# Optimization experiments

Measured on AMD Instinct MI355X. Metric: run time of the kernel, lower is better.

## Reference

```python
import jax, jax.numpy as jnp
import numpy as np

REL_SIZE = 65
TAG_SIZE = 4


def _rope(y):
    # Interleaved rotary position embedding, matching the torch module:
    # cos_pos = cos(theta) repeat_interleave(2), sin_pos = sin(theta) repeat_interleave(2)
    # y2 = (-y1, y0, -y3, y2, ...)
    B, S, H = y.shape
    half = H // 2
    pos = jnp.arange(S, dtype=jnp.float32)[:, None]                      # (S,1)
    inv_freq = jnp.power(10000.0, -2.0 * jnp.arange(half, dtype=jnp.float32) / H)
    theta = pos * inv_freq                                               # (S, half)
    cos = jnp.repeat(jnp.cos(theta), 2, axis=-1)                          # (S, H)
    sin = jnp.repeat(jnp.sin(theta), 2, axis=-1)                          # (S, H)
    yr = y.reshape(B, S, half, 2)
    y2 = jnp.stack([-yr[..., 1], yr[..., 0]], axis=-1).reshape(B, S, H)
    return y * cos + y2 * sin


def setup_inputs() -> dict:
    key = jax.random.key(0)
    k1, k2, k3 = jax.random.split(key, 3)
    B, S, H = 1, 160, 768
    y = jax.random.normal(k1, (B, S, H), dtype=jnp.float32)
    event_idx = jax.random.randint(k2, (B, 16), 0, S)
    W1 = jax.random.normal(k3, (H, 2 * H), dtype=jnp.float32) * 0.02
    b1 = jnp.zeros((H,), dtype=jnp.float32)
    W2 = jax.random.normal(jax.random.fold_in(key, 7), (REL_SIZE * TAG_SIZE, H), dtype=jnp.float32) * 0.02
    b2 = jnp.zeros((REL_SIZE * TAG_SIZE,), dtype=jnp.float32)
    return {"y": y, "event_idx": event_idx, "W1": W1, "b1": b1, "W2": W2, "b2": b2}


def reference(y, event_idx, W1, b1, W2, b2):
    # Eval path (training=False): event_idx unused, dropout = identity, sigmoid applied.
    B, S, H = y.shape
    yrot = _rope(y)
    # Linear(cat(a, b)) is separable: split W1 into the halves acting on a and b.
    Wa, Wb = W1[:, :H], W1[:, H:]
    left = jnp.einsum('bsh,oh->bso', yrot, Wa)                  # contribution of token i (row)
    right = jnp.einsum('bsh,oh->bso', yrot, Wb) + b1            # contribution of token j (col)
    h = jax.nn.relu(left[:, :, None, :] + right[:, None, :, :])  # (B, S, S, H)
    out = jnp.einsum('bijh,oh->bijo', h, W2) + b2               # (B, S, S, 260)
    out = out.reshape(B, S, S, REL_SIZE, TAG_SIZE).transpose(0, 3, 1, 2, 4)  # (B, 65, S, S, 4)
    return jax.nn.sigmoid(out)
```

## Files before the change

kernel.cpp:

```cpp
#include <hip/hip_runtime.h>
#include <hip/hip_bf16.h>
#include <cstdint>

#define SDIM 160
#define HDIM 768
#define HALF 384
#define ODIM 260
#define OPAD 272
#define CHUNK_BYTES 34816
#define WS_SMALL 1155088
#define WS_BIG   3514384

typedef __attribute__((ext_vector_type(8))) short short8;
typedef __attribute__((ext_vector_type(4))) float floatx4;
typedef _Float16 half8 __attribute__((ext_vector_type(8)));

typedef const __attribute__((address_space(1))) unsigned char gl_u8;
typedef __attribute__((address_space(3))) unsigned char lds_u8;

static __device__ __forceinline__ float bf2f(unsigned short u) {
    union { unsigned int i; float f; } v; v.i = ((unsigned int)u) << 16; return v.f;
}
static __device__ __forceinline__ unsigned short f2bf(float x) {
    __hip_bfloat16 h = __float2bfloat16(x);
    return *reinterpret_cast<unsigned short*>(&h);
}
static __device__ __forceinline__ unsigned short f2h(float x) {
    _Float16 h = (_Float16)x;
    return *reinterpret_cast<unsigned short*>(&h);
}
static __device__ __forceinline__ float q(float x) { return bf2f(f2bf(x)); }

__global__ __launch_bounds__(256) void prep_kernel(
    const float* __restrict__ y, const float* __restrict__ W1,
    const float* __restrict__ W2,
    unsigned short* __restrict__ yb, unsigned short* __restrict__ W2b,
    unsigned short* __restrict__ W1b, int do_w1b) {
    int bid = blockIdx.x;
    int t = threadIdx.x;
    if (bid < SDIM) {
        int s = bid;
        for (int p = t; p < HALF; p += 256) {
            float invf = __expf(-(2.0f * (float)p / (float)HDIM) * 9.210340371976184f);
            float th = (float)s * invf;
            float c = cosf(th), sn = sinf(th);
            float y0 = y[s * HDIM + 2 * p], y1 = y[s * HDIM + 2 * p + 1];
            yb[s * HDIM + 2 * p]     = f2bf(y0 * c - y1 * sn);
            yb[s * HDIM + 2 * p + 1] = f2bf(y1 * c + y0 * sn);
        }
    } else if (bid < SDIM + 102) {
        int idx = (bid - SDIM) * 256 + t;
        if (idx < 96 * OPAD) {
            int kg = idx / OPAD, row = idx - kg * OPAD;
            unsigned short o8[8];
            if (row < ODIM) {
                float4 a = *reinterpret_cast<const float4*>(W2 + row * HDIM + kg * 8);
                float4 b = *reinterpret_cast<const float4*>(W2 + row * HDIM + kg * 8 + 4);
                o8[0] = f2h(a.x); o8[1] = f2h(a.y); o8[2] = f2h(a.z); o8[3] = f2h(a.w);
                o8[4] = f2h(b.x); o8[5] = f2h(b.y); o8[6] = f2h(b.z); o8[7] = f2h(b.w);
            } else {
                #pragma unroll
                for (int e = 0; e < 8; ++e) o8[e] = 0;
            }
            *reinterpret_cast<uint4*>(W2b + ((size_t)kg * OPAD + row) * 8) =
                *reinterpret_cast<uint4*>(o8);
        }
    } else if (do_w1b) {
        int idx = (bid - SDIM - 102) * 256 + t;
        int kg = idx / 1536, row = idx - kg * 1536;
        const float* src = (row < 768) ? (W1 + row * 1536 + kg * 8)
                                       : (W1 + (row - 768) * 1536 + 768 + kg * 8);
        float4 a = *reinterpret_cast<const float4*>(src);
        float4 b = *reinterpret_cast<const float4*>(src + 4);
        unsigned short o8[8];
        o8[0] = f2bf(a.x); o8[1] = f2bf(a.y); o8[2] = f2bf(a.z); o8[3] = f2bf(a.w);
        o8[4] = f2bf(b.x); o8[5] = f2bf(b.y); o8[6] = f2bf(b.z); o8[7] = f2bf(b.w);
        *reinterpret_cast<uint4*>(W1b + ((size_t)kg * 1536 + row) * 8) =
            *reinterpret_cast<uint4*>(o8);
    }
}

__global__ __launch_bounds__(64, 2) void lr3_kernel(
    const unsigned short* __restrict__ yb, const unsigned short* __restrict__ W1b,
    const float* __restrict__ b1,
    unsigned short* __restrict__ Lb, unsigned short* __restrict__ Rt) {
    int l = threadIdx.x & 63;
    int l16 = l & 15, qd = l >> 4;
    int mt = blockIdx.x;
    int sq = blockIdx.y;
    int s0 = sq * 16 + l16;

    floatx4 acc = (floatx4){0.0f, 0.0f, 0.0f, 0.0f};

    const unsigned short* yrow0 = yb + s0 * HDIM;

    for (int ks = 0; ks < 24; ++ks) {
        int k = ks * 32 + qd * 8;
        int kg = ks * 4 + qd;
        union { uint4 u; short8 s; } bu0, au;
        bu0.u = *reinterpret_cast<const uint4*>(yrow0 + k);
        au.u = *reinterpret_cast<const uint4*>(
            W1b + ((size_t)kg * 1536 + mt * 16 + l16) * 8);
        acc = __builtin_amdgcn_mfma_f32_16x16x32_bf16(
            au.s, bu0.s, acc, 0, 0, 0);
    }

    int o2 = mt * 16 + qd * 4;
    int s_out = sq * 16 + l16;
    unsigned short out4[4];
    if (o2 < 768) {
        #pragma unroll
        for (int r = 0; r < 4; ++r) out4[r] = f2h(acc[r]);
        *reinterpret_cast<uint2*>(Lb + s_out * HDIM + o2) =
            *reinterpret_cast<uint2*>(out4);
    } else {
        int ob = o2 - 768;
        #pragma unroll
        for (int r = 0; r < 4; ++r)
            out4[r] = f2h(acc[r] + b1[ob + r]);
        *reinterpret_cast<uint2*>(
            Rt + ((size_t)(ob >> 3) * SDIM + s_out) * 8 + (ob & 7)) =
            *reinterpret_cast<uint2*>(out4);
    }
}

__global__ __launch_bounds__(256) void lr_fallback_kernel(
    const unsigned short* __restrict__ yb, const float* __restrict__ W1,
    const float* __restrict__ b1,
    unsigned short* __restrict__ Lb, unsigned short* __restrict__ Rt) {
    int idx = blockIdx.x * 256 + threadIdx.x;
    int s = idx / 1536;
    int o2 = idx - s * 1536;
    const unsigned short* yrow = yb + s * HDIM;
    if (o2 < 768) {
        const float* wp = W1 + o2 * 1536;
        float a0 = 0.0f;
        for (int k = 0; k < HDIM; ++k) a0 += q(wp[k]) * bf2f(yrow[k]);
        Lb[s * HDIM + o2] = f2h(a0);
    } else {
        int ob = o2 - 768;
        const float* wp = W1 + ob * 1536 + 768;
        float a0 = 0.0f;
        for (int k = 0; k < HDIM; ++k) a0 += q(wp[k]) * bf2f(yrow[k]);
        Rt[((size_t)(ob >> 3) * SDIM + s) * 8 + (ob & 7)] = f2h(a0 + b1[ob]);
    }
}

__global__ __launch_bounds__(512) void main_kernel(
    const unsigned short* __restrict__ Lb, const unsigned short* __restrict__ Rt,
    const unsigned short* __restrict__ W2b,
    const float* __restrict__ b2, float* __restrict__ out) {
    __shared__ __align__(16) unsigned char lds[2 * CHUNK_BYTES];

    int w = threadIdx.x >> 6;
    int l = threadIdx.x & 63;
    int l16 = l & 15, qd = l >> 4;
    int jh = w & 1;
    int mq = w >> 1;
    int mt0 = mq * 4;
    int nmt = (mq == 3) ? 5 : 4;
    int i0 = blockIdx.x * 2;
    int j = blockIdx.y * 32 + jh * 16 + l16;

    floatx4 acc[2][5];
    #pragma unroll
    for (int c = 0; c < 2; ++c)
        #pragma unroll
        for (int mtl = 0; mtl < 5; ++mtl)
            acc[c][mtl] = (floatx4){0.0f, 0.0f, 0.0f, 0.0f};

    const unsigned short* Lrow0 = Lb + i0 * HDIM;
    const unsigned short* Lrow1 = Lb + (i0 + 1) * HDIM;
    const unsigned char* wsrc = reinterpret_cast<const unsigned char*>(W2b);

    #pragma unroll
    for (int it = 0; it < 5; ++it) {
        int seg = w + it * 8;
        if (seg < 34) {
            __builtin_amdgcn_global_load_lds(
                (gl_u8*)(wsrc + seg * 1024 + l * 16),
                (lds_u8*)(lds + seg * 1024), 16, 0, 0);
        }
    }
    __syncthreads();

    for (int kc = 0; kc < 12; ++kc) {
        int buf = kc & 1;
        if (kc < 11) {
            const unsigned char* gsrc = wsrc + (kc + 1) * CHUNK_BYTES;
            unsigned char* ldst = lds + (1 - buf) * CHUNK_BYTES;
            #pragma unroll
            for (int it = 0; it < 5; ++it) {
                int seg = w + it * 8;
                if (seg < 34) {
                    __builtin_amdgcn_global_load_lds(
                        (gl_u8*)(gsrc + seg * 1024 + l * 16),
                        (lds_u8*)(ldst + seg * 1024), 16, 0, 0);
                }
            }
        }
        #pragma unroll
        for (int ks = 0; ks < 2; ++ks) {
            int k = kc * 64 + ks * 32 + qd * 8;
            int kg = kc * 8 + ks * 4 + qd;
            half8 bfrag[2];
            union { uint4 u; half8 h; } ru;
            ru.u = *reinterpret_cast<const uint4*>(
                Rt + ((size_t)kg * SDIM + j) * 8);
            #pragma unroll
            for (int c = 0; c < 2; ++c) {
                const unsigned short* Lr = c ? Lrow1 : Lrow0;
                union { uint4 u; half8 h; } lu;
                lu.u = *reinterpret_cast<const uint4*>(Lr + k);
                half8 hv = lu.h + ru.h;
                #pragma unroll
                for (int e = 0; e < 8; ++e)
                    hv[e] = hv[e] > (_Float16)0.0f ? hv[e] : (_Float16)0.0f;
                bfrag[c] = hv;
            }
            int ldsbase = buf * CHUNK_BYTES + ((ks * 4 + qd) * OPAD + l16) * 16;
            #pragma unroll
            for (int mtl = 0; mtl < 5; ++mtl) {
                if (mtl < nmt) {
                    union { uint4 u; half8 h; } au;
                    au.u = *reinterpret_cast<const uint4*>(
                        lds + ldsbase + (mt0 + mtl) * 256);
                    acc[0][mtl] = __builtin_amdgcn_mfma_f32_16x16x32_f16(
                        au.h, bfrag[0], acc[0][mtl], 0, 0, 0);
                    acc[1][mtl] = __builtin_amdgcn_mfma_f32_16x16x32_f16(
                        au.h, bfrag[1], acc[1][mtl], 0, 0, 0);
                }
            }
        }
        __syncthreads();
    }

    #pragma unroll
    for (int c = 0; c < 2; ++c) {
        int i = i0 + c;
        #pragma unroll
        for (int mtl = 0; mtl < 5; ++mtl) {
            if (mtl < nmt) {
                int ob = (mt0 + mtl) * 16 + qd * 4;
                if (ob < ODIM) {
                    float4 bv = *reinterpret_cast<const float4*>(b2 + ob);
                    int rel = ob >> 2;
                    float4 v;
                    v.x = 1.0f / (1.0f + __expf(-(acc[c][mtl][0] + bv.x)));
                    v.y = 1.0f / (1.0f + __expf(-(acc[c][mtl][1] + bv.y)));
                    v.z = 1.0f / (1.0f + __expf(-(acc[c][mtl][2] + bv.z)));
                    v.w = 1.0f / (1.0f + __expf(-(acc[c][mtl][3] + bv.w)));
                    *reinterpret_cast<float4*>(
                        out + (((rel * SDIM) + i) * SDIM + j) * 4) = v;
                }
            }
        }
    }
}

__global__ void ws_too_small_kernel(float* out) { out[0] = 999.0f; }

extern "C" void kernel_launch(void* const* d_in, const int* in_sizes, int n_in,
                              void* d_out, int out_size, void* d_ws, size_t ws_size,
                              hipStream_t stream) {
    const float* y  = (const float*)d_in[0];
    const float* W1 = (const float*)d_in[2];
    const float* b1 = (const float*)d_in[3];
    const float* W2 = (const float*)d_in[4];
    const float* b2 = (const float*)d_in[5];
    float* out = (float*)d_out;

    if (ws_size < (size_t)WS_SMALL) {
        ws_too_small_kernel<<<dim3(1), dim3(1), 0, stream>>>(out);
        return;
    }

    unsigned short* yb  = (unsigned short*)((char*)d_ws + 16);
    unsigned short* Lb  = yb + SDIM * HDIM;
    unsigned short* Rt  = Lb + SDIM * HDIM;
    unsigned short* W2b = Rt + SDIM * HDIM;
    unsigned short* W1b = W2b + 96 * OPAD * 8;

    if (ws_size >= (size_t)WS_BIG) {
        prep_kernel<<<dim3(SDIM + 102 + 576), dim3(256), 0, stream>>>(
            y, W1, W2, yb, W2b, W1b, 1);
        lr3_kernel<<<dim3(96, 10), dim3(64), 0, stream>>>(yb, W1b, b1, Lb, Rt);
        main_kernel<<<dim3(80, 5), dim3(512), 0, stream>>>(Lb, Rt, W2b, b2, out);
    } else {
        prep_kernel<<<dim3(SDIM + 102), dim3(256), 0, stream>>>(
            y, W1, W2, yb, W2b, W1b, 0);
        lr_fallback_kernel<<<dim3(960), dim3(256), 0, stream>>>(yb, W1, b1, Lb, Rt);
        main_kernel<<<dim3(80, 5), dim3(512), 0, stream>>>(Lb, Rt, W2b, b2, out);
    }
}
```

Measured before the change: 109.5 us.

## Triple-buffer W2 LDS staging with vmcnt waits and one barrier per chunk

Moves W2 chunk staging from a double buffer to a three-buffer ring, prefetching two chunks ahead. Explicit s_waitcnt vmcnt counts, tuned per wave to its number of staged loads, replace the end-of-iteration __syncthreads, leaving one raw barrier per iteration. The aim is to hide global-to-LDS latency and cut synchronisation. In exchange, LDS use grows to about 104 KB per block, which may cut resident blocks per CU and split the 400-block grid into more waves. The hand-counted vmcnt values are also fragile against other outstanding vector loads.

```diff
diff --git a/kernel.cpp b/kernel.cpp
--- a/kernel.cpp
+++ b/kernel.cpp
@@ -150,7 +150,7 @@
     const unsigned short* __restrict__ Lb, const unsigned short* __restrict__ Rt,
     const unsigned short* __restrict__ W2b,
     const float* __restrict__ b2, float* __restrict__ out) {
-    __shared__ __align__(16) unsigned char lds[2 * CHUNK_BYTES];
+    __shared__ __align__(16) unsigned char lds[3 * CHUNK_BYTES];
 
     int w = threadIdx.x >> 6;
     int l = threadIdx.x & 63;
@@ -173,32 +173,35 @@
     const unsigned short* Lrow1 = Lb + (i0 + 1) * HDIM;
     const unsigned char* wsrc = reinterpret_cast<const unsigned char*>(W2b);
 
-    #pragma unroll
-    for (int it = 0; it < 5; ++it) {
-        int seg = w + it * 8;
-        if (seg < 34) {
-            __builtin_amdgcn_global_load_lds(
-                (gl_u8*)(wsrc + seg * 1024 + l * 16),
-                (lds_u8*)(lds + seg * 1024), 16, 0, 0);
-        }
-    }
-    __syncthreads();
+    auto STAGE = [&](int ch) {
+        const unsigned char* gsrc = wsrc + ch * CHUNK_BYTES;
+        unsigned char* ldst = lds + (ch % 3) * CHUNK_BYTES;
+        #pragma unroll
+        for (int it = 0; it < 5; ++it) {
+            int seg = w + it * 8;
+            if (seg < 34) {
+                __builtin_amdgcn_global_load_lds(
+                    (gl_u8*)(gsrc + seg * 1024 + l * 16),
+                    (lds_u8*)(ldst + seg * 1024), 16, 0, 0);
+            }
+        }
+    };
+
+    STAGE(0);
+    STAGE(1);
 
     for (int kc = 0; kc < 12; ++kc) {
-        int buf = kc & 1;
-        if (kc < 11) {
-            const unsigned char* gsrc = wsrc + (kc + 1) * CHUNK_BYTES;
-            unsigned char* ldst = lds + (1 - buf) * CHUNK_BYTES;
-            #pragma unroll
-            for (int it = 0; it < 5; ++it) {
-                int seg = w + it * 8;
-                if (seg < 34) {
-                    __builtin_amdgcn_global_load_lds(
-                        (gl_u8*)(gsrc + seg * 1024 + l * 16),
-                        (lds_u8*)(ldst + seg * 1024), 16, 0, 0);
-                }
-            }
-        }
+        if (kc == 11) {
+            asm volatile("s_waitcnt vmcnt(0)" ::: "memory");
+        } else if (w < 2) {
+            asm volatile("s_waitcnt vmcnt(5)" ::: "memory");
+        } else {
+            asm volatile("s_waitcnt vmcnt(4)" ::: "memory");
+        }
+        __builtin_amdgcn_s_barrier();
+        if (kc < 10) STAGE(kc + 2);
+
+        int bufbase = (kc % 3) * CHUNK_BYTES;
         #pragma unroll
         for (int ks = 0; ks < 2; ++ks) {
             int k = kc * 64 + ks * 32 + qd * 8;
@@ -218,7 +221,7 @@
                     hv[e] = hv[e] > (_Float16)0.0f ? hv[e] : (_Float16)0.0f;
                 bfrag[c] = hv;
             }
-            int ldsbase = buf * CHUNK_BYTES + ((ks * 4 + qd) * OPAD + l16) * 16;
+            int ldsbase = bufbase + ((ks * 4 + qd) * OPAD + l16) * 16;
             #pragma unroll
             for (int mtl = 0; mtl < 5; ++mtl) {
                 if (mtl < nmt) {
@@ -232,7 +235,6 @@
                 }
             }
         }
-        __syncthreads();
     }
 
     #pragma unroll
```

Measured after the change: 123.4 us. +12.7%, slower.
